# Kernel tuning notes

Hardware: AMD Instinct MI355X
Metric: run time of the kernel (lower is better)

The kernel has to match this reference:

```python
import jax, jax.numpy as jnp
import numpy as np

B, N, C, H = 4, 1024, 1024, 16
HD = C // H
SCALE = HD ** -0.5


def _init_linear(key, out_dim, in_dim):
    # torch nn.Linear default init: U(-1/sqrt(in), 1/sqrt(in)) for weight and bias
    kw, kb = jax.random.split(key)
    bound = 1.0 / np.sqrt(in_dim)
    W = jax.random.uniform(kw, (out_dim, in_dim), jnp.float32, -bound, bound)
    b = jax.random.uniform(kb, (out_dim,), jnp.float32, -bound, bound)
    return W, b


def setup_inputs() -> dict:
    key = jax.random.key(0)
    ks = jax.random.split(key, 5)
    x = jax.random.normal(ks[0], (B, N, C), jnp.float32)
    # NdLinear qkv: Linear(N->N) along seq axis, then Linear(C->3C) along channel axis
    Wq0, bq0 = _init_linear(ks[1], N, N)
    Wq1, bq1 = _init_linear(ks[2], 3 * C, C)
    # NdLinear proj: Linear(N->N) along seq axis, then Linear(C->C) along channel axis
    Wp0, bp0 = _init_linear(ks[3], N, N)
    Wp1, bp1 = _init_linear(ks[4], C, C)
    return {"x": x, "Wq0": Wq0, "bq0": bq0, "Wq1": Wq1, "bq1": bq1,
            "Wp0": Wp0, "bp0": bp0, "Wp1": Wp1, "bp1": bp1}


def _ndlinear(x, W0, b0, W1, b1):
    # NdLinear over (seq, channel): apply Linear along axis 1, then axis 2.
    # torch Linear: y = x @ W.T + b
    x = jnp.einsum('bnc,mn->bmc', x, W0) + b0[None, :, None]   # seq axis
    x = jnp.einsum('bnc,dc->bnd', x, W1) + b1                  # channel axis
    return x


def reference(x, Wq0, bq0, Wq1, bq1, Wp0, bp0, Wp1, bp1):
    qkv = _ndlinear(x, Wq0, bq0, Wq1, bq1)                     # (B, N, 3C)
    qkv = qkv.reshape(B, N, 3, H, HD).transpose(2, 0, 3, 1, 4) # (3, B, H, N, HD)
    q, k, v = qkv[0], qkv[1], qkv[2]
    attn = jnp.einsum('bhnd,bhmd->bhnm', q, k) * SCALE         # (B, H, N, N)
    attn = jax.nn.softmax(attn, axis=-1)
    out = jnp.einsum('bhnm,bhmd->bhnd', attn, v)               # (B, H, N, HD)
    out = out.transpose(0, 2, 1, 3).reshape(B, N, C)
    out = _ndlinear(out, Wp0, bp0, Wp1, bp1)
    return out
```

## Files before the change

kernel.cpp:

```cpp
#include <hip/hip_runtime.h>
#include <hip/hip_bf16.h>
#include <stdint.h>

typedef __bf16 bf16;
typedef __bf16 bf16x4 __attribute__((ext_vector_type(4)));
typedef __bf16 bf16x8 __attribute__((ext_vector_type(8)));
typedef float f32x4 __attribute__((ext_vector_type(4)));

#define B_ 4
#define N_ 1024
#define C_ 1024
#define H_ 16
#define MEG (1u << 20)

__device__ __forceinline__ uint32_t lds_off(const void* p) {
    return (uint32_t)(uintptr_t)p;
}
__device__ __forceinline__ void g2l16(const void* g, uint32_t lds_byte) {
    __builtin_amdgcn_global_load_lds(
        (const __attribute__((address_space(1))) unsigned int*)(uintptr_t)g,
        (__attribute__((address_space(3))) unsigned int*)(uintptr_t)lds_byte,
        16, 0, 0);
}

__global__ __launch_bounds__(256) void cvt4_k(
    const float* __restrict__ s0, bf16* __restrict__ d0,
    const float* __restrict__ s1, bf16* __restrict__ d1,
    const float* __restrict__ s2, bf16* __restrict__ d2,
    const float* __restrict__ s3, bf16* __restrict__ d3) {
    int bid = blockIdx.x;
    const float* s; bf16* d; int base;
    if (bid < 512)       { s = s0; d = d0; base = 0; }
    else if (bid < 2048) { s = s1; d = d1; base = 512; }
    else if (bid < 2560) { s = s2; d = d2; base = 2048; }
    else                 { s = s3; d = d3; base = 2560; }
    int i = ((bid - base) * 256 + threadIdx.x) * 8;
    float4 a = *(const float4*)(s + i);
    float4 b = *(const float4*)(s + i + 4);
    bf16x8 r;
    r[0] = (bf16)a.x; r[1] = (bf16)a.y; r[2] = (bf16)a.z; r[3] = (bf16)a.w;
    r[4] = (bf16)b.x; r[5] = (bf16)b.y; r[6] = (bf16)b.z; r[7] = (bf16)b.w;
    *(bf16x8*)(d + i) = r;
}

__global__ __launch_bounds__(256) void xpose_k(const float* __restrict__ x,
                                               bf16* __restrict__ xT) {
    __shared__ bf16 t[64][66];
    const int tid = threadIdx.x;
    const int b = blockIdx.z, n0 = blockIdx.y * 64, c0 = blockIdx.x * 64;
    {
        int nl = tid >> 2, seg = tid & 3;
        const float* src = x + ((size_t)b * N_ + n0 + nl) * C_ + c0 + seg * 16;
#pragma unroll
        for (int i = 0; i < 4; ++i) {
            float4 v = *(const float4*)(src + i * 4);
            t[nl][seg * 16 + i * 4 + 0] = (bf16)v.x;
            t[nl][seg * 16 + i * 4 + 1] = (bf16)v.y;
            t[nl][seg * 16 + i * 4 + 2] = (bf16)v.z;
            t[nl][seg * 16 + i * 4 + 3] = (bf16)v.w;
        }
    }
    __syncthreads();
    {
        int cl = tid >> 2, seg = tid & 3;
        bf16* dst = xT + ((size_t)b * C_ + c0 + cl) * N_ + n0 + seg * 16;
        bf16x8 o0, o1;
#pragma unroll
        for (int j = 0; j < 8; ++j) o0[j] = t[seg * 16 + j][cl];
#pragma unroll
        for (int j = 0; j < 8; ++j) o1[j] = t[seg * 16 + 8 + j][cl];
        *(bf16x8*)dst = o0;
        *(bf16x8*)(dst + 8) = o1;
    }
}

template <int BIAS, bool OF32>
__global__ __launch_bounds__(512) void gemm_k(
    const bf16* __restrict__ A, const bf16* __restrict__ Bm,
    const float* __restrict__ bias, void* __restrict__ Cv,
    int M, int Nn, int K, long long sA, long long sB, long long sC)
{
    __shared__ bf16 smem[2][2][128 * 64];

    const int tid = threadIdx.x;
    const int lane = tid & 63, wid = tid >> 6;
    const int lr = lane & 15, lg = lane >> 4;
    const int wr = wid >> 2, wc = wid & 3;
    const int m0 = blockIdx.y * 128, n0 = blockIdx.x * 128;

    const bf16* Ab = A + (size_t)blockIdx.z * sA;
    const bf16* Bb = Bm + (size_t)blockIdx.z * sB;

    const uint32_t a_lds0 = lds_off(&smem[0][0][0]);
    const uint32_t b_lds0 = lds_off(&smem[0][1][0]);
    const uint32_t bufstride = 2 * 128 * 64 * 2;

    auto stage = [&](int kt, int buf) {
#pragma unroll
        for (int half = 0; half < 2; ++half) {
            int it = tid + half * 512;
            int r = it >> 3, ch = it & 7;
            int sch = ch ^ (r & 7);
            g2l16(Ab + (size_t)(m0 + r) * K + kt * 64 + sch * 8,
                  a_lds0 + buf * bufstride + it * 16);
            g2l16(Bb + (size_t)(n0 + r) * K + kt * 64 + sch * 8,
                  b_lds0 + buf * bufstride + it * 16);
        }
    };

    f32x4 acc[4][2];
#pragma unroll
    for (int i = 0; i < 4; ++i)
#pragma unroll
        for (int j = 0; j < 2; ++j) { f32x4 z = {0.f,0.f,0.f,0.f}; acc[i][j] = z; }

    stage(0, 0);
    __syncthreads();

    const int nt = K >> 6;
    for (int t = 0; t < nt; ++t) {
        int buf = t & 1;
        if (t + 1 < nt) stage(t + 1, buf ^ 1);
        const bf16* As = &smem[buf][0][0];
        const bf16* Bs = &smem[buf][1][0];
#pragma unroll
        for (int s = 0; s < 2; ++s) {
            bf16x8 af[4], bfr[2];
#pragma unroll
            for (int mi = 0; mi < 4; ++mi) {
                int row = wr * 64 + mi * 16 + lr;
                int slot = (s * 4 + lg) ^ (row & 7);
                af[mi] = *(const bf16x8*)(As + row * 64 + slot * 8);
            }
#pragma unroll
            for (int ni = 0; ni < 2; ++ni) {
                int row = wc * 32 + ni * 16 + lr;
                int slot = (s * 4 + lg) ^ (row & 7);
                bfr[ni] = *(const bf16x8*)(Bs + row * 64 + slot * 8);
            }
#pragma unroll
            for (int mi = 0; mi < 4; ++mi)
#pragma unroll
                for (int ni = 0; ni < 2; ++ni)
                    acc[mi][ni] = __builtin_amdgcn_mfma_f32_16x16x32_bf16(
                        af[mi], bfr[ni], acc[mi][ni], 0, 0, 0);
        }
        __syncthreads();
    }

#pragma unroll
    for (int mi = 0; mi < 4; ++mi)
#pragma unroll
        for (int ni = 0; ni < 2; ++ni)
#pragma unroll
            for (int r = 0; r < 4; ++r) {
                int row = m0 + wr * 64 + mi * 16 + lg * 4 + r;
                int col = n0 + wc * 32 + ni * 16 + lr;
                float bv = (BIAS == 0) ? bias[row] : bias[col];
                float v = acc[mi][ni][r] + bv;
                if constexpr (OF32)
                    ((float*)Cv + (size_t)blockIdx.z * sC)[(size_t)row * Nn + col] = v;
                else
                    ((bf16*)Cv + (size_t)blockIdx.z * sC)[(size_t)row * Nn + col] = (bf16)v;
            }
}

__global__ __launch_bounds__(512) void attn_k(
    const bf16* __restrict__ qkv, bf16* __restrict__ aoT)
{
    __shared__ bf16 Ks[2][4096];
    __shared__ bf16 Vs[2][4096];
    __shared__ bf16 pbuf[8][16][72];

    const int tid = threadIdx.x;
    const int lane = tid & 63, wid = tid >> 6;
    const int lr = lane & 15, lg = lane >> 4;
    const int bid = blockIdx.x;
    const int qt = bid >> 6, hb = bid & 63;
    const int b = hb >> 4, h = hb & 15;
    const int qrow0 = qt * 128 + wid * 16;
    const int hoff = h * 64;
    const bf16* qkvb = qkv + (size_t)b * (N_ * 3 * C_);

    bf16x8 qf[2];
#pragma unroll
    for (int kk = 0; kk < 2; ++kk)
        qf[kk] = *(const bf16x8*)(qkvb + (size_t)(qrow0 + lr) * 3072 +
                                  hoff + kk * 32 + lg * 8);

    const uint32_t ks0 = lds_off(&Ks[0][0]);
    const int vd = tid & 63, vkg = tid >> 6;

    auto stageK = [&](int kt, int buf) {
        int key = tid >> 3, ch = tid & 7;
        int sch = ch ^ (key & 7);
        g2l16(qkvb + (size_t)(kt * 64 + key) * 3072 + C_ + hoff + sch * 8,
              ks0 + buf * 8192 + tid * 16);
    };
    auto loadV = [&](int kt) -> bf16x8 {
        const bf16* base = qkvb + 2 * C_ + hoff + vd;
        bf16x8 v;
#pragma unroll
        for (int j = 0; j < 8; ++j)
            v[j] = base[(size_t)(kt * 64 + vkg * 8 + j) * 3072];
        return v;
    };
    auto writeV = [&](bf16x8 v, int buf) {
        *(bf16x8*)(&Vs[buf][vd * 64 + ((vkg ^ (vd & 7)) * 8)]) = v;
    };

    float lsum[4] = {0.f, 0.f, 0.f, 0.f};
    f32x4 o[4];
#pragma unroll
    for (int i = 0; i < 4; ++i) { f32x4 z = {0.f,0.f,0.f,0.f}; o[i] = z; }

    stageK(0, 0);
    writeV(loadV(0), 0);
    __syncthreads();

    for (int kt = 0; kt < 16; ++kt) {
        int buf = kt & 1;
        bf16x8 vnext;
        if (kt + 1 < 16) {
            stageK(kt + 1, buf ^ 1);
            vnext = loadV(kt + 1);
        }

        f32x4 s[4];
#pragma unroll
        for (int st = 0; st < 4; ++st) {
            f32x4 z = {0.f, 0.f, 0.f, 0.f};
#pragma unroll
            for (int kk = 0; kk < 2; ++kk) {
                int row = st * 16 + lr;
                int slot = (kk * 4 + lg) ^ (row & 7);
                bf16x8 kf = *(const bf16x8*)(&Ks[buf][row * 64 + slot * 8]);
                z = __builtin_amdgcn_mfma_f32_16x16x32_bf16(qf[kk], kf, z, 0, 0, 0);
            }
            s[st] = z;
        }

#pragma unroll
        for (int st = 0; st < 4; ++st)
#pragma unroll
            for (int r = 0; r < 4; ++r) {
                float e = __expf(s[st][r] * 0.125f);
                bf16 pb = (bf16)e;
                lsum[r] += (float)pb;
                pbuf[wid][lg * 4 + r][st * 16 + lr] = pb;
            }

        bf16x8 pf[2];
        pf[0] = *(const bf16x8*)(&pbuf[wid][lr][lg * 8]);
        pf[1] = *(const bf16x8*)(&pbuf[wid][lr][32 + lg * 8]);

#pragma unroll
        for (int dt = 0; dt < 4; ++dt) {
            int row = dt * 16 + lr;
            bf16x8 v0 = *(const bf16x8*)(&Vs[buf][row * 64 + ((lg ^ (lr & 7)) * 8)]);
            bf16x8 v1 = *(const bf16x8*)(&Vs[buf][row * 64 + (((4 + lg) ^ (lr & 7)) * 8)]);
            o[dt] = __builtin_amdgcn_mfma_f32_16x16x32_bf16(pf[0], v0, o[dt], 0, 0, 0);
            o[dt] = __builtin_amdgcn_mfma_f32_16x16x32_bf16(pf[1], v1, o[dt], 0, 0, 0);
        }

        if (kt + 1 < 16) writeV(vnext, buf ^ 1);
        __syncthreads();
    }

#pragma unroll
    for (int m = 1; m < 16; m <<= 1)
#pragma unroll
        for (int r = 0; r < 4; ++r)
            lsum[r] += __shfl_xor(lsum[r], m, 64);

#pragma unroll
    for (int dt = 0; dt < 4; ++dt) {
        bf16x4 ov;
#pragma unroll
        for (int r = 0; r < 4; ++r) ov[r] = (bf16)(o[dt][r] / lsum[r]);
        size_t c = (size_t)b * C_ + hoff + dt * 16 + lr;
        *(bf16x4*)(aoT + c * N_ + qrow0 + lg * 4) = ov;
    }
}

extern "C" void kernel_launch(void* const* d_in, const int* in_sizes, int n_in,
                              void* d_out, int out_size, void* d_ws, size_t ws_size,
                              hipStream_t stream) {
    (void)in_sizes; (void)n_in; (void)out_size; (void)ws_size;
    const float* x   = (const float*)d_in[0];
    const float* Wq0 = (const float*)d_in[1];
    const float* bq0 = (const float*)d_in[2];
    const float* Wq1 = (const float*)d_in[3];
    const float* bq1 = (const float*)d_in[4];
    const float* Wp0 = (const float*)d_in[5];
    const float* bp0 = (const float*)d_in[6];
    const float* Wp1 = (const float*)d_in[7];
    const float* bp1 = (const float*)d_in[8];

    bf16* ws   = (bf16*)d_ws;
    bf16* xT   = ws;
    bf16* Wq0b = ws + 4 * MEG;
    bf16* Wq1b = ws + 5 * MEG;
    bf16* Wp0b = ws + 8 * MEG;
    bf16* Wp1b = ws + 9 * MEG;
    bf16* y1   = ws + 10 * MEG;
    bf16* y2   = ws + 14 * MEG;
    bf16* aoT  = y1;
    bf16* z1   = y2;
    float* outp = (float*)d_out;

    const long long s1M = (long long)N_ * C_;

    cvt4_k<<<dim3(3072), 256, 0, stream>>>(Wq0, Wq0b, Wq1, Wq1b,
                                           Wp0, Wp0b, Wp1, Wp1b);
    xpose_k<<<dim3(16, 16, 4), 256, 0, stream>>>(x, xT);

    gemm_k<0, false><<<dim3(8, 8, 4), 512, 0, stream>>>(
        Wq0b, xT, bq0, y1, 1024, 1024, 1024, 0LL, s1M, s1M);
    gemm_k<1, false><<<dim3(24, 32, 1), 512, 0, stream>>>(
        y1, Wq1b, bq1, y2, 4096, 3072, 1024, 0LL, 0LL, 0LL);
    attn_k<<<dim3(512), 512, 0, stream>>>(y2, aoT);
    gemm_k<0, false><<<dim3(8, 8, 4), 512, 0, stream>>>(
        Wp0b, aoT, bp0, z1, 1024, 1024, 1024, 0LL, s1M, s1M);
    gemm_k<1, true><<<dim3(8, 32, 1), 512, 0, stream>>>(
        z1, Wp1b, bp1, outp, 4096, 1024, 1024, 0LL, 0LL, 0LL);
}
```

Baseline: 123.9 us.

## Fold softmax scale into Q, use exp2, transpose S tile for vectorized P stores

Pre-scales Q by scale*log2(e) so the softmax uses a raw exp2 with no per-element multiply. Swaps the MFMA operand order so each lane holds a key column of S, which allows packed bf16x4 writes of P into a swizzled LDS buffer instead of scalar stores. Row sums become one scalar per lane, reduced with two shuffles, and the final divide becomes a reciprocal multiply. It also raises wave priority around the MFMA blocks; the trade is rounding Q to bf16 after scaling and summing unrounded exponentials.

```diff
diff --git a/kernel.cpp b/kernel.cpp
--- a/kernel.cpp
+++ b/kernel.cpp
@@ -170,7 +170,7 @@
 {
     __shared__ bf16 Ks[2][4096];
     __shared__ bf16 Vs[2][4096];
-    __shared__ bf16 pbuf[8][16][72];
+    __shared__ bf16 pbuf[8][1024];
 
     const int tid = threadIdx.x;
     const int lane = tid & 63, wid = tid >> 6;
@@ -184,9 +184,13 @@
 
     bf16x8 qf[2];
 #pragma unroll
-    for (int kk = 0; kk < 2; ++kk)
+    for (int kk = 0; kk < 2; ++kk) {
         qf[kk] = *(const bf16x8*)(qkvb + (size_t)(qrow0 + lr) * 3072 +
                                   hoff + kk * 32 + lg * 8);
+#pragma unroll
+        for (int j = 0; j < 8; ++j)
+            qf[kk][j] = (bf16)((float)qf[kk][j] * 0.18033688f);
+    }
 
     const uint32_t ks0 = lds_off(&Ks[0][0]);
     const int vd = tid & 63, vkg = tid >> 6;
@@ -209,10 +213,13 @@
         *(bf16x8*)(&Vs[buf][vd * 64 + ((vkg ^ (vd & 7)) * 8)]) = v;
     };
 
-    float lsum[4] = {0.f, 0.f, 0.f, 0.f};
+    float lsum = 0.f;
     f32x4 o[4];
 #pragma unroll
     for (int i = 0; i < 4; ++i) { f32x4 z = {0.f,0.f,0.f,0.f}; o[i] = z; }
+
+    char* prow = (char*)&pbuf[wid][0] + lr * 128;
+    const int swz = (lr & 7) << 4;
 
     stageK(0, 0);
     writeV(loadV(0), 0);
@@ -227,6 +234,7 @@
         }
 
         f32x4 s[4];
+        __builtin_amdgcn_s_setprio(1);
 #pragma unroll
         for (int st = 0; st < 4; ++st) {
             f32x4 z = {0.f, 0.f, 0.f, 0.f};
@@ -235,25 +243,29 @@
                 int row = st * 16 + lr;
                 int slot = (kk * 4 + lg) ^ (row & 7);
                 bf16x8 kf = *(const bf16x8*)(&Ks[buf][row * 64 + slot * 8]);
-                z = __builtin_amdgcn_mfma_f32_16x16x32_bf16(qf[kk], kf, z, 0, 0, 0);
+                z = __builtin_amdgcn_mfma_f32_16x16x32_bf16(kf, qf[kk], z, 0, 0, 0);
             }
             s[st] = z;
         }
-
-#pragma unroll
-        for (int st = 0; st < 4; ++st)
+        __builtin_amdgcn_s_setprio(0);
+
+#pragma unroll
+        for (int st = 0; st < 4; ++st) {
+            bf16x4 w;
 #pragma unroll
             for (int r = 0; r < 4; ++r) {
-                float e = __expf(s[st][r] * 0.125f);
-                bf16 pb = (bf16)e;
-                lsum[r] += (float)pb;
-                pbuf[wid][lg * 4 + r][st * 16 + lr] = pb;
-            }
+                float e = __builtin_amdgcn_exp2f(s[st][r]);
+                w[r] = (bf16)e;
+                lsum += e;
+            }
+            *(bf16x4*)(prow + ((st * 32 + lg * 8) ^ swz)) = w;
+        }
 
         bf16x8 pf[2];
-        pf[0] = *(const bf16x8*)(&pbuf[wid][lr][lg * 8]);
-        pf[1] = *(const bf16x8*)(&pbuf[wid][lr][32 + lg * 8]);
-
+        pf[0] = *(const bf16x8*)(prow + ((lg * 16) ^ swz));
+        pf[1] = *(const bf16x8*)(prow + ((64 + lg * 16) ^ swz));
+
+        __builtin_amdgcn_s_setprio(1);
 #pragma unroll
         for (int dt = 0; dt < 4; ++dt) {
             int row = dt * 16 + lr;
@@ -262,22 +274,24 @@
             o[dt] = __builtin_amdgcn_mfma_f32_16x16x32_bf16(pf[0], v0, o[dt], 0, 0, 0);
             o[dt] = __builtin_amdgcn_mfma_f32_16x16x32_bf16(pf[1], v1, o[dt], 0, 0, 0);
         }
+        __builtin_amdgcn_s_setprio(0);
 
         if (kt + 1 < 16) writeV(vnext, buf ^ 1);
         __syncthreads();
     }
 
-#pragma unroll
-    for (int m = 1; m < 16; m <<= 1)
-#pragma unroll
-        for (int r = 0; r < 4; ++r)
-            lsum[r] += __shfl_xor(lsum[r], m, 64);
+    lsum += __shfl_xor(lsum, 16, 64);
+    lsum += __shfl_xor(lsum, 32, 64);
+    float rtot = 1.0f / lsum;
+    float rcpo[4];
+#pragma unroll
+    for (int r = 0; r < 4; ++r) rcpo[r] = __shfl(rtot, lg * 4 + r, 64);
 
 #pragma unroll
     for (int dt = 0; dt < 4; ++dt) {
         bf16x4 ov;
 #pragma unroll
-        for (int r = 0; r < 4; ++r) ov[r] = (bf16)(o[dt][r] / lsum[r]);
+        for (int r = 0; r < 4; ++r) ov[r] = (bf16)(o[dt][r] * rcpo[r]);
         size_t c = (size_t)b * C_ + hoff + dt * 16 + lr;
         *(bf16x4*)(aoT + c * N_ + qrow0 + lg * 4) = ov;
     }
```

Result: faster. 121.1 us (-2.3%).
